# Kernel optimization log

Hardware: AMD Instinct MI355X
Metric: run time of the kernel (lower is better)

## Reference

```python
import jax, jax.numpy as jnp
import numpy as np

NUM_GROUPS = 32
EPS = 1e-6


def group_norm(x, gamma, beta):
    # x: [B, C, H, W]
    B, C, H, W = x.shape
    xg = x.reshape(B, NUM_GROUPS, C // NUM_GROUPS, H, W)
    mu = jnp.mean(xg, axis=(2, 3, 4), keepdims=True)
    var = jnp.var(xg, axis=(2, 3, 4), keepdims=True)
    xg = (xg - mu) * jax.lax.rsqrt(var + EPS)
    x = xg.reshape(B, C, H, W)
    return x * gamma[None, :, None, None] + beta[None, :, None, None]


def conv1x1(x, w, b):
    # x: [B, C, H, W], w: [O, C], b: [O]
    return jnp.einsum('bchw,oc->bohw', x, w) + b[None, :, None, None]


def setup_inputs() -> dict:
    key = jax.random.key(0)
    C = 512
    B, H, W = 4, 64, 64
    ks = jax.random.split(key, 10)
    s = 1.0 / np.sqrt(C)
    inp = {
        'x': jax.random.normal(ks[0], (B, C, H, W), dtype=jnp.float32),
        'gamma': jnp.ones((C,), dtype=jnp.float32),
        'beta': jnp.zeros((C,), dtype=jnp.float32),
        'wq': jax.random.normal(ks[1], (C, C), dtype=jnp.float32) * s,
        'bq': jnp.zeros((C,), dtype=jnp.float32),
        'wk': jax.random.normal(ks[2], (C, C), dtype=jnp.float32) * s,
        'bk': jnp.zeros((C,), dtype=jnp.float32),
        'wv': jax.random.normal(ks[3], (C, C), dtype=jnp.float32) * s,
        'bv': jnp.zeros((C,), dtype=jnp.float32),
        'wo': jax.random.normal(ks[4], (C, C), dtype=jnp.float32) * s,
        'bo': jnp.zeros((C,), dtype=jnp.float32),
    }
    return inp


def reference(x, gamma, beta, wq, bq, wk, bk, wv, bv, wo, bo):
    B, C, H, W = x.shape
    h = group_norm(x, gamma, beta)
    q = conv1x1(h, wq, bq).reshape(B, C, H * W)  # [B, C, S]
    k = conv1x1(h, wk, bk).reshape(B, C, H * W)
    v = conv1x1(h, wv, bv).reshape(B, C, H * W)
    scale = C ** (-0.5)
    # scores[b, S, s] = sum_c q[b, c, S] * k[b, c, s]
    w = jnp.einsum('bcS,bcs->bSs', q, k) * scale
    w = jax.nn.softmax(w, axis=-1)
    # out[b, c, S] = sum_s w[b, S, s] * v[b, c, s]
    hattn = jnp.einsum('bSs,bcs->bcS', w, v).reshape(B, C, H, W)
    out = conv1x1(hattn, wo, bo)
    return x + out
```

## Files before the change

kernel.cpp:

```cpp
#include <hip/hip_runtime.h>

#define B_   4
#define C_   512
#define S_   4096
#define G_   32
#define CPG_ 16
#define EPS_ 1e-6f

typedef unsigned short u16;
typedef __bf16 bf16x8 __attribute__((ext_vector_type(8)));
typedef float  f32x4  __attribute__((ext_vector_type(4)));

__device__ __forceinline__ u16 f2bf(float f) {
  unsigned u = __float_as_uint(f);
  u += 0x7fffu + ((u >> 16) & 1u);
  return (u16)(u >> 16);
}
__device__ __forceinline__ float bf2f(u16 h) {
  return __uint_as_float((unsigned)h << 16);
}

__device__ __forceinline__ void g2lds16(const void* g, void* l) {
  __builtin_amdgcn_global_load_lds(
      (const __attribute__((address_space(1))) void*)g,
      (__attribute__((address_space(3))) void*)l, 16, 0, 0);
}

#define BAR()    __builtin_amdgcn_s_barrier()
#define SCHED0() __builtin_amdgcn_sched_barrier(0)
#define WAITV4   asm volatile("s_waitcnt vmcnt(4)" ::: "memory")
#define WAITV0   asm volatile("s_waitcnt vmcnt(0)" ::: "memory")
#define LGKM0    asm volatile("s_waitcnt lgkmcnt(0)" ::: "memory")

__device__ __forceinline__ void xcd_swz(int& bx, int& by, int& bz) {
  const int gx = gridDim.x, gy = gridDim.y;
  const int nwg = gx * gy * (int)gridDim.z;
  const int flat = blockIdx.x + gx * (blockIdx.y + gy * blockIdx.z);
  const int q = nwg >> 3;
  const int nf = (flat & 7) * q + (flat >> 3);
  bx = nf % gx;
  const int r = nf / gx;
  by = r % gy;
  bz = r / gy;
}

__global__ __launch_bounds__(256) void f32_to_bf16(const float* __restrict__ in,
                                                   u16* __restrict__ out, int n) {
  int i = blockIdx.x * 256 + threadIdx.x;
  if (i < n) out[i] = f2bf(in[i]);
}

__global__ __launch_bounds__(256) void concat_bias(const float* __restrict__ a,
                                                   const float* __restrict__ b,
                                                   float* __restrict__ o) {
  int i = blockIdx.x * 256 + threadIdx.x;
  o[i] = (i < 512) ? a[i] : b[i - 512];
}

__global__ __launch_bounds__(256) void reduce_l(const float* __restrict__ p,
                                                float* __restrict__ lr) {
  const int i = blockIdx.x * 256 + threadIdx.x;
  const int b = i >> 12, row = i & 4095;
  float s = 0.f;
#pragma unroll
  for (int jb = 0; jb < 16; ++jb) s += p[((size_t)(b * 16 + jb) << 12) + row];
  lr[i] = 1.f / s;
}

__global__ __launch_bounds__(256) void add_scale_bf16(const u16* __restrict__ a,
                                                      const u16* __restrict__ b,
                                                      const float* __restrict__ lr,
                                                      u16* __restrict__ o) {
  const int i = blockIdx.x * 256 + threadIdx.x;
  const size_t i8 = (size_t)i * 8;
  const int bi = (int)(i8 >> 21);
  const int row = (int)(i8 >> 9) & 4095;
  const float sc = lr[bi * 4096 + row];
  const uint4 ua = ((const uint4*)a)[i];
  const uint4 ub = ((const uint4*)b)[i];
  const unsigned* pa = (const unsigned*)&ua;
  const unsigned* pb = (const unsigned*)&ub;
  unsigned r[4];
#pragma unroll
  for (int k = 0; k < 4; ++k) {
    const float lo = (bf2f((u16)(pa[k] & 0xffffu)) + bf2f((u16)(pb[k] & 0xffffu))) * sc;
    const float hi = (bf2f((u16)(pa[k] >> 16)) + bf2f((u16)(pb[k] >> 16))) * sc;
    r[k] = (unsigned)f2bf(lo) | ((unsigned)f2bf(hi) << 16);
  }
  ((uint4*)o)[i] = *(const uint4*)r;
}

__global__ __launch_bounds__(256) void gn_stats(const float* __restrict__ x,
                                                float* __restrict__ stats) {
  const int bg = blockIdx.x;
  const float4* p4 = (const float4*)(x + (size_t)bg * (CPG_ * S_));
  float s = 0.f, ss = 0.f;
  const int tid = threadIdx.x;
  for (int i = tid; i < CPG_ * S_ / 4; i += 256) {
    float4 v = p4[i];
    s  += v.x + v.y + v.z + v.w;
    ss += v.x * v.x + v.y * v.y + v.z * v.z + v.w * v.w;
  }
#pragma unroll
  for (int o = 32; o; o >>= 1) { s += __shfl_xor(s, o, 64); ss += __shfl_xor(ss, o, 64); }
  __shared__ float sm[8];
  const int wid = tid >> 6, lane = tid & 63;
  if (lane == 0) { sm[wid * 2] = s; sm[wid * 2 + 1] = ss; }
  __syncthreads();
  if (tid == 0) {
    s  = sm[0] + sm[2] + sm[4] + sm[6];
    ss = sm[1] + sm[3] + sm[5] + sm[7];
    const float inv = 1.f / (float)(CPG_ * S_);
    float mu = s * inv;
    float var = ss * inv - mu * mu;
    stats[bg * 2]     = mu;
    stats[bg * 2 + 1] = rsqrtf(var + EPS_);
  }
}

__global__ __launch_bounds__(256) void gn_apply_t(const float* __restrict__ x,
                                                  const float* __restrict__ gamma,
                                                  const float* __restrict__ beta,
                                                  const float* __restrict__ stats,
                                                  u16* __restrict__ ht) {
  __shared__ float tile[32][33];
  const int b = blockIdx.z, c0 = blockIdx.y * 32, s0 = blockIdx.x * 32;
  const int tx = threadIdx.x, ty = threadIdx.y;
#pragma unroll
  for (int i = 0; i < 4; ++i) {
    const int c  = c0 + ty + i * 8;
    const float mu = stats[(b * G_ + (c >> 4)) * 2];
    const float rs = stats[(b * G_ + (c >> 4)) * 2 + 1];
    const float v  = x[((size_t)b * C_ + c) * S_ + s0 + tx];
    tile[ty + i * 8][tx] = (v - mu) * rs * gamma[c] + beta[c];
  }
  __syncthreads();
#pragma unroll
  for (int i = 0; i < 4; ++i) {
    const int s = s0 + ty + i * 8;
    ht[((size_t)b * S_ + s) * C_ + c0 + tx] = f2bf(tile[tx][ty + i * 8]);
  }
}

template <int BIAS_MODE, int ZMODE, int SMAX>
__global__ __launch_bounds__(512, 2) void gemm8p(
    const u16* __restrict__ Ag, int lda, long sA,
    const u16* __restrict__ Bg, int ldb, long sB,
    u16* __restrict__ Cg, int ldc, long sC,
    const float* __restrict__ bias, float alpha, int K,
    float* __restrict__ smx) {
  __shared__ u16 As[2][2][8192];
  __shared__ u16 Bs[2][2][8192];
  __shared__ float ps[4][256];
  int bx, by, bz;
  xcd_swz(bx, by, bz);
  const u16 *A, *Bm;
  u16* Cb;
  if (ZMODE == 0) {
    A = Ag + (size_t)bz * sA; Bm = Bg + (size_t)bz * sB; Cb = Cg + (size_t)bz * sC;
  } else {
    const int b = bz >> 1, kh = bz & 1;
    A  = Ag + (size_t)b * 16777216 + (size_t)kh * 2048;
    Bm = Bg + (size_t)b * 4096 + (size_t)kh * 2048;
    Cb = Cg + (size_t)kh * 8388608 + (size_t)b * 2097152;
  }
  const int bm = by * 256, bn = bx * 256;
  const int tid = threadIdx.x;
  const int wid = tid >> 6, lane = tid & 63;
  const int wm = (wid >> 2) * 16, wn = (wid & 3) * 16;
  const int lr = lane & 15, lh = lane >> 4;
  const int x7 = lr & 7;
  const int g0 = (lh ^ x7) * 8, g1 = ((4 | lh) ^ x7) * 8;

  const int sg = (lane & 7) ^ ((lane >> 3) & 7);
  const u16* Abase = A  + (size_t)(bm + wid * 8 + (lane >> 3)) * lda + sg * 8;
  const u16* Bbase = Bm + (size_t)(bn + wid * 8 + (lane >> 3)) * ldb + sg * 8;

#define STGA(D, H, T) do {                                                   \
    const u16* _s = Abase + (size_t)((H) * 128) * lda + (size_t)(T) * 64;    \
    g2lds16(_s,                    &As[D][H][wid * 512]);                    \
    g2lds16(_s + (size_t)64 * lda, &As[D][H][4096 + wid * 512]);             \
  } while (0)
#define STGB(D, H, T) do {                                                   \
    const u16* _s = Bbase + (size_t)((H) * 128) * ldb + (size_t)(T) * 64;    \
    g2lds16(_s,                    &Bs[D][H][wid * 512]);                    \
    g2lds16(_s + (size_t)64 * ldb, &Bs[D][H][4096 + wid * 512]);             \
  } while (0)

  float bias_v[4] = {0.f, 0.f, 0.f, 0.f};
  if (BIAS_MODE == 1) {
#pragma unroll
    for (int g = 0; g < 4; ++g) bias_v[g] = bias[bn + wn + g * 64 + lr];
  }
  SCHED0();

  f32x4 acc[8][4];
  const f32x4 zero = {0.f, 0.f, 0.f, 0.f};
#pragma unroll
  for (int i = 0; i < 8; ++i)
#pragma unroll
    for (int j = 0; j < 4; ++j) acc[i][j] = zero;

  bf16x8 a_[4][2], b_[4][2];

#define RDA(D, AH) do {                                                      \
    _Pragma("unroll") for (int i = 0; i < 4; ++i) {                          \
      const int _o = (wm + i * 32 + lr) * 64;                                \
      a_[i][0] = *(const bf16x8*)&As[D][AH][_o + g0];                        \
      a_[i][1] = *(const bf16x8*)&As[D][AH][_o + g1];                        \
    } } while (0)
#define RDB(D, BH) do {                                                      \
    _Pragma("unroll") for (int j = 0; j < 2; ++j) {                          \
      const int _o = (wn + j * 64 + lr) * 64;                                \
      b_[(BH) * 2 + j][0] = *(const bf16x8*)&Bs[D][BH][_o + g0];             \
      b_[(BH) * 2 + j][1] = *(const bf16x8*)&Bs[D][BH][_o + g1];             \
    } } while (0)
#define MM(AH, BH) do {                                                      \
    __builtin_amdgcn_s_setprio(1);                                           \
    _Pragma("unroll") for (int i = 0; i < 4; ++i)                            \
    _Pragma("unroll") for (int j = 0; j < 2; ++j) {                          \
      acc[(AH) * 4 + i][(BH) * 2 + j] = __builtin_amdgcn_mfma_f32_16x16x32_bf16( \
          a_[i][0], b_[(BH) * 2 + j][0], acc[(AH) * 4 + i][(BH) * 2 + j], 0, 0, 0); \
      acc[(AH) * 4 + i][(BH) * 2 + j] = __builtin_amdgcn_mfma_f32_16x16x32_bf16( \
          a_[i][1], b_[(BH) * 2 + j][1], acc[(AH) * 4 + i][(BH) * 2 + j], 0, 0, 0); \
    }                                                                        \
    __builtin_amdgcn_s_setprio(0);                                           \
  } while (0)
#define MID() SCHED0(); BAR(); LGKM0; SCHED0()

  STGA(0, 0, 0); STGB(0, 1, 0); STGA(0, 1, 0); STGB(0, 0, 0);
  STGA(1, 0, 1); STGB(1, 1, 1);
  WAITV4;
  BAR();

  const int nt = K >> 6;
  for (int i = 0; i < nt / 2; ++i) {
    const int t1 = 2 * i + 1, t2 = 2 * i + 2, t3 = 2 * i + 3;
    const bool s2 = t2 < nt, s3 = t3 < nt;
    RDA(0, 0); RDB(0, 0);
    STGB(1, 0, t1);
    MID(); MM(0, 0); BAR();
    RDB(0, 1);
    STGA(1, 1, t1);
    MID(); MM(0, 1); BAR();
    RDA(0, 1);
    if (s2) STGA(0, 0, t2);
    MID(); MM(1, 1); BAR();
    if (s2) STGB(0, 1, t2);
    MID(); MM(1, 0);
    if (s2) { WAITV4; } else { WAITV0; }
    BAR();
    RDA(1, 0); RDB(1, 0);
    if (s2) STGA(0, 1, t2);
    MID(); MM(0, 0); BAR();
    RDB(1, 1);
    if (s2) STGB(0, 0, t2);
    MID(); MM(0, 1); BAR();
    RDA(1, 1);
    if (s3) STGA(1, 0, t3);
    MID(); MM(1, 1); BAR();
    if (s3) STGB(1, 1, t3);
    MID(); MM(1, 0);
    if (s3) { WAITV4; }
    BAR();
  }
#undef STGA
#undef STGB
#undef RDA
#undef RDB
#undef MM
#undef MID
  SCHED0();

  if (SMAX) {
    float rs[8][4];
#pragma unroll
    for (int f = 0; f < 8; ++f) {
      const int row0 = bm + wm + f * 32 + lh * 4;
#pragma unroll
      for (int r = 0; r < 4; ++r) rs[f][r] = 0.f;
#pragma unroll
      for (int g = 0; g < 4; ++g) {
        const int col = bn + wn + g * 64 + lr;
#pragma unroll
        for (int r = 0; r < 4; ++r) {
          const float e = __expf(acc[f][g][r] * alpha);
          rs[f][r] += e;
          Cb[(size_t)(row0 + r) * ldc + col] = f2bf(e);
        }
      }
#pragma unroll
      for (int r = 0; r < 4; ++r) {
        float v = rs[f][r];
        v += __shfl_xor(v, 1, 64);
        v += __shfl_xor(v, 2, 64);
        v += __shfl_xor(v, 4, 64);
        v += __shfl_xor(v, 8, 64);
        rs[f][r] = v;
      }
    }
#pragma unroll
    for (int f = 0; f < 8; ++f)
#pragma unroll
      for (int r = 0; r < 4; ++r)
        if (lr == ((f << 1) | (r >> 1)))
          ps[wid & 3][wm + f * 32 + lh * 4 + r] = rs[f][r];
    __syncthreads();
    if (tid < 256) {
      const float tot = ps[0][tid] + ps[1][tid] + ps[2][tid] + ps[3][tid];
      smx[((size_t)(bz * 16 + bx) << 12) + bm + tid] = tot;
    }
  } else {
#pragma unroll
    for (int f = 0; f < 8; ++f) {
      const int row0 = bm + wm + f * 32 + lh * 4;
#pragma unroll
      for (int g = 0; g < 4; ++g) {
        const int col = bn + wn + g * 64 + lr;
#pragma unroll
        for (int r = 0; r < 4; ++r)
          Cb[(size_t)(row0 + r) * ldc + col] = f2bf(acc[f][g][r] * alpha + bias_v[g]);
      }
    }
  }
}

#define GBM 128
#define GBN 128
#define GBK 64

template <int BIAS_MODE, int OUT_MODE>
__global__ __launch_bounds__(256) void gemm_abT(
    const u16* __restrict__ Ag, int lda, long sA,
    const u16* __restrict__ Bg, int ldb, long sB,
    void* __restrict__ Cg, int ldc, long sC,
    const float* __restrict__ bias, float alpha,
    const float* __restrict__ xres, int K) {
  __shared__ u16 As[GBM * GBK];
  __shared__ u16 Bs[GBN * GBK];
  const int bz = blockIdx.z;
  const u16* A    = Ag + (size_t)bz * sA;
  const u16* Bmat = Bg + (size_t)bz * sB;
  const int bm = blockIdx.y * GBM, bn = blockIdx.x * GBN;
  const int tid = threadIdx.x;
  const int wid = tid >> 6, lane = tid & 63;
  const int wm = (wid >> 1) * 64, wn = (wid & 1) * 64;
  const int lr = lane & 15, lh = lane >> 4;
  const int srow = lane >> 3, scol = (lane & 7) * 8;

  f32x4 acc[4][4];
  const f32x4 zero = {0.f, 0.f, 0.f, 0.f};
#pragma unroll
  for (int i = 0; i < 4; ++i)
#pragma unroll
    for (int j = 0; j < 4; ++j) acc[i][j] = zero;

  for (int k0 = 0; k0 < K; k0 += GBK) {
    __syncthreads();
#pragma unroll
    for (int i = 0; i < 4; ++i) {
      const int chunk = wid * 4 + i;
      const int row   = chunk * 8 + srow;
      g2lds16(A    + (size_t)(bm + row) * lda + (k0 + scol), &As[chunk * 512]);
      g2lds16(Bmat + (size_t)(bn + row) * ldb + (k0 + scol), &Bs[chunk * 512]);
    }
    __syncthreads();
#pragma unroll
    for (int ks = 0; ks < 2; ++ks) {
      bf16x8 a_[4], b_[4];
#pragma unroll
      for (int m = 0; m < 4; ++m)
        a_[m] = *(const bf16x8*)&As[(wm + m * 16 + lr) * GBK + ks * 32 + lh * 8];
#pragma unroll
      for (int n = 0; n < 4; ++n)
        b_[n] = *(const bf16x8*)&Bs[(wn + n * 16 + lr) * GBK + ks * 32 + lh * 8];
#pragma unroll
      for (int m = 0; m < 4; ++m)
#pragma unroll
        for (int n = 0; n < 4; ++n)
          acc[m][n] = __builtin_amdgcn_mfma_f32_16x16x32_bf16(a_[m], b_[n], acc[m][n], 0, 0, 0);
    }
  }

  if (OUT_MODE == 0) {
    u16* Cb = (u16*)Cg + (size_t)bz * sC;
#pragma unroll
    for (int m = 0; m < 4; ++m) {
      const int row0 = bm + wm + m * 16 + lh * 4;
#pragma unroll
      for (int n = 0; n < 4; ++n) {
        const int col = bn + wn + n * 16 + lr;
        float bn_ = (BIAS_MODE == 1) ? bias[col] : 0.f;
#pragma unroll
        for (int r = 0; r < 4; ++r) {
          float bb = (BIAS_MODE == 2) ? bias[row0 + r] : bn_;
          Cb[(size_t)(row0 + r) * ldc + col] = f2bf(acc[m][n][r] * alpha + bb);
        }
      }
    }
  } else {
    float* Ob = (float*)Cg;
#pragma unroll
    for (int m = 0; m < 4; ++m) {
      const int row0 = bm + wm + m * 16 + lh * 4;
#pragma unroll
      for (int n = 0; n < 4; ++n) {
        const int col = bn + wn + n * 16 + lr;
        const int bb = col >> 12, sp = col & (S_ - 1);
#pragma unroll
        for (int r = 0; r < 4; ++r) {
          const int o = row0 + r;
          const size_t idx = ((size_t)bb * C_ + o) * S_ + sp;
          Ob[idx] = acc[m][n][r] * alpha + bias[o] + xres[idx];
        }
      }
    }
  }
}

extern "C" void kernel_launch(void* const* d_in, const int* in_sizes, int n_in,
                              void* d_out, int out_size, void* d_ws, size_t ws_size,
                              hipStream_t stream) {
  const float* x     = (const float*)d_in[0];
  const float* gamma = (const float*)d_in[1];
  const float* beta  = (const float*)d_in[2];
  const float* wq = (const float*)d_in[3];
  const float* bq = (const float*)d_in[4];
  const float* wk = (const float*)d_in[5];
  const float* bk = (const float*)d_in[6];
  const float* wv = (const float*)d_in[7];
  const float* bv = (const float*)d_in[8];
  const float* wo = (const float*)d_in[9];
  const float* bo = (const float*)d_in[10];
  float* out = (float*)d_out;

  char* ws = (char*)d_ws;
  float* stats = (float*)ws;
  u16* wqb = (u16*)(ws + 1024);
  u16* wkb = wqb + 262144;
  u16* wvb = wkb + 262144;
  u16* wob = wvb + 262144;
  float* bqk = (float*)(wob + 262144);
  u16* ht  = (u16*)((char*)bqk + 4096);
  u16* qkt = ht + 8388608;
  u16* vv  = qkt + 16777216;
  u16* sc  = vv + 8388608;
  float* partials = (float*)(sc + 67108864);
  float* Lr = partials + 262144;

  f32_to_bf16<<<1024, 256, 0, stream>>>(wq, wqb, 262144);
  f32_to_bf16<<<1024, 256, 0, stream>>>(wk, wkb, 262144);
  f32_to_bf16<<<1024, 256, 0, stream>>>(wv, wvb, 262144);
  f32_to_bf16<<<1024, 256, 0, stream>>>(wo, wob, 262144);
  concat_bias<<<4, 256, 0, stream>>>(bq, bk, bqk);

  gn_stats<<<128, 256, 0, stream>>>(x, stats);
  gn_apply_t<<<dim3(128, 16, 4), dim3(32, 8), 0, stream>>>(x, gamma, beta, stats, ht);

  gemm8p<1, 0, 0><<<dim3(4, 64, 1), 512, 0, stream>>>(ht, 512, 0, wqb, 512, 0,
                                                      qkt, 1024, 0, bqk, 1.f, 512, nullptr);
  gemm_abT<2, 0><<<dim3(128, 4, 1), 256, 0, stream>>>(wvb, 512, 0, ht, 512, 0,
                                                      vv, 16384, 0, bv, 1.f, nullptr, 512);
  gemm8p<0, 0, 1><<<dim3(16, 16, 4), 512, 0, stream>>>(qkt, 1024, 4194304, qkt + 512, 1024, 4194304,
                                                       sc, 4096, 16777216, nullptr,
                                                       0.04419417382415922f, 512, partials);
  reduce_l<<<64, 256, 0, stream>>>(partials, Lr);
  gemm8p<0, 1, 0><<<dim3(2, 16, 8), 512, 0, stream>>>(sc, 4096, 0, vv, 16384, 0,
                                                      qkt, 512, 0, nullptr, 1.f, 2048, nullptr);
  add_scale_bf16<<<4096, 256, 0, stream>>>(qkt, qkt + 8388608, Lr, vv);
  gemm_abT<2, 1><<<dim3(128, 4, 1), 256, 0, stream>>>(wob, 512, 0, vv, 512, 0,
                                                      out, 0, 0, bo, 1.f, x, 512);
}
```

Measured before the change: 293.8 us.

## Rewrite 256x256 GEMM mainloop with 4-slot K32 LDS ring and 128x64 warp tiles

```diff
diff --git a/kernel.cpp b/kernel.cpp
--- a/kernel.cpp
+++ b/kernel.cpp
@@ -30,7 +30,6 @@
 #define SCHED0() __builtin_amdgcn_sched_barrier(0)
 #define WAITV4   asm volatile("s_waitcnt vmcnt(4)" ::: "memory")
 #define WAITV0   asm volatile("s_waitcnt vmcnt(0)" ::: "memory")
-#define LGKM0    asm volatile("s_waitcnt lgkmcnt(0)" ::: "memory")
 
 __device__ __forceinline__ void xcd_swz(int& bx, int& by, int& bz) {
   const int gx = gridDim.x, gy = gridDim.y;
@@ -63,7 +62,10 @@
   const int b = i >> 12, row = i & 4095;
   float s = 0.f;
 #pragma unroll
-  for (int jb = 0; jb < 16; ++jb) s += p[((size_t)(b * 16 + jb) << 12) + row];
+  for (int jb = 0; jb < 16; ++jb)
+#pragma unroll
+    for (int w = 0; w < 4; ++w)
+      s += p[(((size_t)(b * 16 + jb) * 4 + w) << 12) + row];
   lr[i] = 1.f / s;
 }
 
@@ -142,16 +144,42 @@
   }
 }
 
+#define STAGE_A(T, KS) do {                                                  \
+    const int _sl = (2 * (T) + (KS)) & 3;                                    \
+    const size_t _ko = (size_t)(T) * 64 + (KS) * 32;                         \
+    g2lds16(Asrc + _ko,  &As[_sl][wid * 512]);                               \
+    g2lds16(Asrc2 + _ko, &As[_sl][4096 + wid * 512]);                        \
+  } while (0)
+#define STAGE_B(T, KS) do {                                                  \
+    const int _sl = (2 * (T) + (KS)) & 3;                                    \
+    const size_t _ko = (size_t)(T) * 64 + (KS) * 32;                         \
+    g2lds16(Bsrc + _ko,  &Bs[_sl][wid * 512]);                               \
+    g2lds16(Bsrc2 + _ko, &Bs[_sl][4096 + wid * 512]);                        \
+  } while (0)
+#define LDB4(SL)                                                             \
+  _Pragma("unroll") for (int i = 0; i < 4; ++i)                              \
+      bfr[i] = *(const bf16x8*)&Bs[(SL)][bbase + i * 512];
+#define LDA4(SL, MH)                                                         \
+  _Pragma("unroll") for (int i = 0; i < 4; ++i)                              \
+      af[i] = *(const bf16x8*)&As[(SL)][abase + ((MH) * 4 + i) * 512];
+#define MFMA16(MH) do {                                                      \
+    __builtin_amdgcn_s_setprio(1);                                           \
+    _Pragma("unroll") for (int mi = 0; mi < 4; ++mi)                         \
+    _Pragma("unroll") for (int ni = 0; ni < 4; ++ni)                         \
+      acc[(MH) * 4 + mi][ni] = __builtin_amdgcn_mfma_f32_16x16x32_bf16(      \
+          af[mi], bfr[ni], acc[(MH) * 4 + mi][ni], 0, 0, 0);                 \
+    __builtin_amdgcn_s_setprio(0);                                           \
+  } while (0)
+
 template <int BIAS_MODE, int ZMODE, int SMAX>
-__global__ __launch_bounds__(512, 2) void gemm8p(
+__global__ __launch_bounds__(512, 2) void gemm256(
     const u16* __restrict__ Ag, int lda, long sA,
     const u16* __restrict__ Bg, int ldb, long sB,
     u16* __restrict__ Cg, int ldc, long sC,
     const float* __restrict__ bias, float alpha, int K,
     float* __restrict__ smx) {
-  __shared__ u16 As[2][2][8192];
-  __shared__ u16 Bs[2][2][8192];
-  __shared__ float ps[4][256];
+  __shared__ u16 As[4][8192];
+  __shared__ u16 Bs[4][8192];
   int bx, by, bz;
   xcd_swz(bx, by, bz);
   const u16 *A, *Bm;
@@ -167,30 +195,24 @@
   const int bm = by * 256, bn = bx * 256;
   const int tid = threadIdx.x;
   const int wid = tid >> 6, lane = tid & 63;
-  const int wm = (wid >> 2) * 16, wn = (wid & 3) * 16;
+  const int wm = (wid >> 2) * 128, wn = (wid & 3) * 64;
   const int lr = lane & 15, lh = lane >> 4;
-  const int x7 = lr & 7;
-  const int g0 = (lh ^ x7) * 8, g1 = ((4 | lh) ^ x7) * 8;
-
-  const int sg = (lane & 7) ^ ((lane >> 3) & 7);
-  const u16* Abase = A  + (size_t)(bm + wid * 8 + (lane >> 3)) * lda + sg * 8;
-  const u16* Bbase = Bm + (size_t)(bn + wid * 8 + (lane >> 3)) * ldb + sg * 8;
-
-#define STGA(D, H, T) do {                                                   \
-    const u16* _s = Abase + (size_t)((H) * 128) * lda + (size_t)(T) * 64;    \
-    g2lds16(_s,                    &As[D][H][wid * 512]);                    \
-    g2lds16(_s + (size_t)64 * lda, &As[D][H][4096 + wid * 512]);             \
-  } while (0)
-#define STGB(D, H, T) do {                                                   \
-    const u16* _s = Bbase + (size_t)((H) * 128) * ldb + (size_t)(T) * 64;    \
-    g2lds16(_s,                    &Bs[D][H][wid * 512]);                    \
-    g2lds16(_s + (size_t)64 * ldb, &Bs[D][H][4096 + wid * 512]);             \
-  } while (0)
+
+  const int srow = wid * 16 + (lane >> 2);
+  const int sg   = (lane & 3) ^ ((srow >> 1) & 3);
+  const u16* Asrc  = A  + (size_t)(bm + srow) * lda + sg * 8;
+  const u16* Asrc2 = Asrc + (size_t)128 * lda;
+  const u16* Bsrc  = Bm + (size_t)(bn + srow) * ldb + sg * 8;
+  const u16* Bsrc2 = Bsrc + (size_t)128 * ldb;
+
+  const int swz   = (lh ^ ((lr >> 1) & 3)) << 3;
+  const int abase = (wm + lr) * 32 + swz;
+  const int bbase = (wn + lr) * 32 + swz;
 
   float bias_v[4] = {0.f, 0.f, 0.f, 0.f};
   if (BIAS_MODE == 1) {
 #pragma unroll
-    for (int g = 0; g < 4; ++g) bias_v[g] = bias[bn + wn + g * 64 + lr];
+    for (int nf = 0; nf < 4; ++nf) bias_v[nf] = bias[bn + wn + nf * 16 + lr];
   }
   SCHED0();
 
@@ -201,125 +223,77 @@
 #pragma unroll
     for (int j = 0; j < 4; ++j) acc[i][j] = zero;
 
-  bf16x8 a_[4][2], b_[4][2];
-
-#define RDA(D, AH) do {                                                      \
-    _Pragma("unroll") for (int i = 0; i < 4; ++i) {                          \
-      const int _o = (wm + i * 32 + lr) * 64;                                \
-      a_[i][0] = *(const bf16x8*)&As[D][AH][_o + g0];                        \
-      a_[i][1] = *(const bf16x8*)&As[D][AH][_o + g1];                        \
-    } } while (0)
-#define RDB(D, BH) do {                                                      \
-    _Pragma("unroll") for (int j = 0; j < 2; ++j) {                          \
-      const int _o = (wn + j * 64 + lr) * 64;                                \
-      b_[(BH) * 2 + j][0] = *(const bf16x8*)&Bs[D][BH][_o + g0];             \
-      b_[(BH) * 2 + j][1] = *(const bf16x8*)&Bs[D][BH][_o + g1];             \
-    } } while (0)
-#define MM(AH, BH) do {                                                      \
-    __builtin_amdgcn_s_setprio(1);                                           \
-    _Pragma("unroll") for (int i = 0; i < 4; ++i)                            \
-    _Pragma("unroll") for (int j = 0; j < 2; ++j) {                          \
-      acc[(AH) * 4 + i][(BH) * 2 + j] = __builtin_amdgcn_mfma_f32_16x16x32_bf16( \
-          a_[i][0], b_[(BH) * 2 + j][0], acc[(AH) * 4 + i][(BH) * 2 + j], 0, 0, 0); \
-      acc[(AH) * 4 + i][(BH) * 2 + j] = __builtin_amdgcn_mfma_f32_16x16x32_bf16( \
-          a_[i][1], b_[(BH) * 2 + j][1], acc[(AH) * 4 + i][(BH) * 2 + j], 0, 0, 0); \
-    }                                                                        \
-    __builtin_amdgcn_s_setprio(0);                                           \
-  } while (0)
-#define MID() SCHED0(); BAR(); LGKM0; SCHED0()
-
-  STGA(0, 0, 0); STGB(0, 1, 0); STGA(0, 1, 0); STGB(0, 0, 0);
-  STGA(1, 0, 1); STGB(1, 1, 1);
-  WAITV4;
-  BAR();
+  STAGE_A(0, 0); STAGE_B(0, 0); STAGE_A(0, 1); STAGE_B(0, 1);
 
   const int nt = K >> 6;
-  for (int i = 0; i < nt / 2; ++i) {
-    const int t1 = 2 * i + 1, t2 = 2 * i + 2, t3 = 2 * i + 3;
-    const bool s2 = t2 < nt, s3 = t3 < nt;
-    RDA(0, 0); RDB(0, 0);
-    STGB(1, 0, t1);
-    MID(); MM(0, 0); BAR();
-    RDB(0, 1);
-    STGA(1, 1, t1);
-    MID(); MM(0, 1); BAR();
-    RDA(0, 1);
-    if (s2) STGA(0, 0, t2);
-    MID(); MM(1, 1); BAR();
-    if (s2) STGB(0, 1, t2);
-    MID(); MM(1, 0);
-    if (s2) { WAITV4; } else { WAITV0; }
-    BAR();
-    RDA(1, 0); RDB(1, 0);
-    if (s2) STGA(0, 1, t2);
-    MID(); MM(0, 0); BAR();
-    RDB(1, 1);
-    if (s2) STGB(0, 0, t2);
-    MID(); MM(0, 1); BAR();
-    RDA(1, 1);
-    if (s3) STGA(1, 0, t3);
-    MID(); MM(1, 1); BAR();
-    if (s3) STGB(1, 1, t3);
-    MID(); MM(1, 0);
-    if (s3) { WAITV4; }
-    BAR();
-  }
-#undef STGA
-#undef STGB
-#undef RDA
-#undef RDB
-#undef MM
-#undef MID
+  for (int t = 0; t < nt; ++t) {
+    const int s0 = (2 * t) & 3, s1 = s0 + 1;
+    const bool pre = (t + 1 < nt);
+    bf16x8 bfr[4], af[4];
+    WAITV4;
+    BAR(); SCHED0();
+    LDB4(s0);
+    LDA4(s0, 0);
+    if (pre) STAGE_A(t + 1, 0);
+    MFMA16(0);
+    BAR(); SCHED0();
+    LDA4(s0, 1);
+    if (pre) STAGE_B(t + 1, 0);
+    MFMA16(1);
+    if (pre) { WAITV4; } else { WAITV0; }
+    BAR(); SCHED0();
+    LDB4(s1);
+    LDA4(s1, 0);
+    if (pre) STAGE_A(t + 1, 1);
+    MFMA16(0);
+    BAR(); SCHED0();
+    LDA4(s1, 1);
+    if (pre) STAGE_B(t + 1, 1);
+    MFMA16(1);
+  }
   SCHED0();
 
   if (SMAX) {
     float rs[8][4];
 #pragma unroll
-    for (int f = 0; f < 8; ++f) {
-      const int row0 = bm + wm + f * 32 + lh * 4;
-#pragma unroll
-      for (int r = 0; r < 4; ++r) rs[f][r] = 0.f;
-#pragma unroll
-      for (int g = 0; g < 4; ++g) {
-        const int col = bn + wn + g * 64 + lr;
+    for (int mf = 0; mf < 8; ++mf) {
+      const int row0 = bm + wm + mf * 16 + lh * 4;
+#pragma unroll
+      for (int r = 0; r < 4; ++r) rs[mf][r] = 0.f;
+#pragma unroll
+      for (int nf = 0; nf < 4; ++nf) {
+        const int col = bn + wn + nf * 16 + lr;
 #pragma unroll
         for (int r = 0; r < 4; ++r) {
-          const float e = __expf(acc[f][g][r] * alpha);
-          rs[f][r] += e;
+          const float e = __expf(acc[mf][nf][r] * alpha);
+          rs[mf][r] += e;
           Cb[(size_t)(row0 + r) * ldc + col] = f2bf(e);
         }
       }
+    }
+#pragma unroll
+    for (int mf = 0; mf < 8; ++mf)
 #pragma unroll
       for (int r = 0; r < 4; ++r) {
-        float v = rs[f][r];
+        float v = rs[mf][r];
         v += __shfl_xor(v, 1, 64);
         v += __shfl_xor(v, 2, 64);
         v += __shfl_xor(v, 4, 64);
         v += __shfl_xor(v, 8, 64);
-        rs[f][r] = v;
+        if (lr == 0)
+          smx[(((size_t)bz * 16 + bx) * 4 + (wid & 3)) * 4096 +
+              bm + wm + mf * 16 + lh * 4 + r] = v;
       }
-    }
-#pragma unroll
-    for (int f = 0; f < 8; ++f)
-#pragma unroll
-      for (int r = 0; r < 4; ++r)
-        if (lr == ((f << 1) | (r >> 1)))
-          ps[wid & 3][wm + f * 32 + lh * 4 + r] = rs[f][r];
-    __syncthreads();
-    if (tid < 256) {
-      const float tot = ps[0][tid] + ps[1][tid] + ps[2][tid] + ps[3][tid];
-      smx[((size_t)(bz * 16 + bx) << 12) + bm + tid] = tot;
-    }
   } else {
 #pragma unroll
-    for (int f = 0; f < 8; ++f) {
-      const int row0 = bm + wm + f * 32 + lh * 4;
-#pragma unroll
-      for (int g = 0; g < 4; ++g) {
-        const int col = bn + wn + g * 64 + lr;
+    for (int mf = 0; mf < 8; ++mf) {
+      const int row0 = bm + wm + mf * 16 + lh * 4;
+#pragma unroll
+      for (int nf = 0; nf < 4; ++nf) {
+        const int col = bn + wn + nf * 16 + lr;
 #pragma unroll
         for (int r = 0; r < 4; ++r)
-          Cb[(size_t)(row0 + r) * ldc + col] = f2bf(acc[f][g][r] * alpha + bias_v[g]);
+          Cb[(size_t)(row0 + r) * ldc + col] = f2bf(acc[mf][nf][r] * alpha + bias_v[nf]);
       }
     }
   }
@@ -445,8 +419,8 @@
   u16* qkt = ht + 8388608;
   u16* vv  = qkt + 16777216;
   u16* sc  = vv + 8388608;
-  float* partials = (float*)(sc + 67108864);
-  float* Lr = partials + 262144;
+  float* partials = (float*)ht;
+  float* Lr = partials + 1048576;
 
   f32_to_bf16<<<1024, 256, 0, stream>>>(wq, wqb, 262144);
   f32_to_bf16<<<1024, 256, 0, stream>>>(wk, wkb, 262144);
@@ -457,16 +431,16 @@
   gn_stats<<<128, 256, 0, stream>>>(x, stats);
   gn_apply_t<<<dim3(128, 16, 4), dim3(32, 8), 0, stream>>>(x, gamma, beta, stats, ht);
 
-  gemm8p<1, 0, 0><<<dim3(4, 64, 1), 512, 0, stream>>>(ht, 512, 0, wqb, 512, 0,
-                                                      qkt, 1024, 0, bqk, 1.f, 512, nullptr);
+  gemm256<1, 0, 0><<<dim3(4, 64, 1), 512, 0, stream>>>(ht, 512, 0, wqb, 512, 0,
+                                                       qkt, 1024, 0, bqk, 1.f, 512, nullptr);
   gemm_abT<2, 0><<<dim3(128, 4, 1), 256, 0, stream>>>(wvb, 512, 0, ht, 512, 0,
                                                       vv, 16384, 0, bv, 1.f, nullptr, 512);
-  gemm8p<0, 0, 1><<<dim3(16, 16, 4), 512, 0, stream>>>(qkt, 1024, 4194304, qkt + 512, 1024, 4194304,
-                                                       sc, 4096, 16777216, nullptr,
-                                                       0.04419417382415922f, 512, partials);
+  gemm256<0, 0, 1><<<dim3(16, 16, 4), 512, 0, stream>>>(qkt, 1024, 4194304, qkt + 512, 1024, 4194304,
+                                                        sc, 4096, 16777216, nullptr,
+                                                        0.04419417382415922f, 512, partials);
   reduce_l<<<64, 256, 0, stream>>>(partials, Lr);
-  gemm8p<0, 1, 0><<<dim3(2, 16, 8), 512, 0, stream>>>(sc, 4096, 0, vv, 16384, 0,
-                                                      qkt, 512, 0, nullptr, 1.f, 2048, nullptr);
+  gemm256<0, 1, 0><<<dim3(2, 16, 8), 512, 0, stream>>>(sc, 4096, 0, vv, 16384, 0,
+                                                       qkt, 512, 0, nullptr, 1.f, 2048, nullptr);
   add_scale_bf16<<<4096, 256, 0, stream>>>(qkt, qkt + 8388608, Lr, vv);
   gemm_abT<2, 1><<<dim3(128, 4, 1), 256, 0, stream>>>(wob, 512, 0, vv, 512, 0,
                                                       out, 0, 0, bo, 1.f, x, 512);
```

Result: slower. 310.3 us (+5.6%).
